# Kernel optimization log

Hardware: AMD Instinct MI355X
Metric: run time of the kernel (lower is better)

Reference implementation:

```python
import jax, jax.numpy as jnp
import numpy as np

N_ENT = 100000   # n_entities
N_HE = 20000     # n_hyperedges
D = 128          # in_dim == out_dim
NNZ_A = 3200000  # nnz of A_in (avg degree 32)
NNZ_H = 1000000  # nnz of each hyperedge incidence matrix


def spmm(rows, cols, vals, x, n_rows):
    """COO sparse (n_rows, n_cols) @ dense x (n_cols, d) -> (n_rows, d)."""
    return jax.ops.segment_sum(vals[:, None] * x[cols], rows, num_segments=n_rows)


def setup_inputs() -> dict:
    key = jax.random.key(0)
    ks = jax.random.split(key, 20)
    ri = lambda k, n, hi: jax.random.randint(k, (n,), 0, hi, dtype=jnp.int32)
    rv = lambda k, n: jax.random.uniform(k, (n,), dtype=jnp.float32) * 0.1
    inp = {
        "ego": jax.random.normal(ks[0], (N_ENT, D), dtype=jnp.float32),
        "A_rows": ri(ks[1], NNZ_A, N_ENT),
        "A_cols": ri(ks[2], NNZ_A, N_ENT),
        "A_vals": rv(ks[3], NNZ_A),
        "p1_rows": ri(ks[4], NNZ_H, N_HE),
        "p1_cols": ri(ks[5], NNZ_H, N_ENT),
        "p1_vals": rv(ks[6], NNZ_H),
        "p2_rows": ri(ks[7], NNZ_H, N_ENT),
        "p2_cols": ri(ks[8], NNZ_H, N_HE),
        "p2_vals": rv(ks[9], NNZ_H),
        "l1_rows": ri(ks[10], NNZ_H, N_HE),
        "l1_cols": ri(ks[11], NNZ_H, N_ENT),
        "l1_vals": rv(ks[12], NNZ_H),
        "l2_rows": ri(ks[13], NNZ_H, N_ENT),
        "l2_cols": ri(ks[14], NNZ_H, N_HE),
        "l2_vals": rv(ks[15], NNZ_H),
        "W1": jax.random.normal(ks[16], (D, D), dtype=jnp.float32) * (1.0 / np.sqrt(D)),
        "b1": jnp.zeros((D,), dtype=jnp.float32),
        "W2": jax.random.normal(ks[17], (D, D), dtype=jnp.float32) * (1.0 / np.sqrt(D)),
        "b2": jnp.zeros((D,), dtype=jnp.float32),
    }
    return inp


def reference(ego, A_rows, A_cols, A_vals,
              p1_rows, p1_cols, p1_vals, p2_rows, p2_cols, p2_vals,
              l1_rows, l1_cols, l1_vals, l2_rows, l2_cols, l2_vals,
              W1, b1, W2, b2):
    # side = A_in @ ego
    side = spmm(A_rows, A_cols, A_vals, ego, N_ENT)
    # proj = norm_proj2 @ (norm_proj1 @ ego)
    proj = spmm(p2_rows, p2_cols, p2_vals,
                spmm(p1_rows, p1_cols, p1_vals, ego, N_HE), N_ENT)
    # lib = norm_lib2 @ (norm_lib1 @ ego)
    lib = spmm(l2_rows, l2_cols, l2_vals,
               spmm(l1_rows, l1_cols, l1_vals, ego, N_HE), N_ENT)
    side = side + proj + lib
    # bi-interaction: LeakyReLU(Linear(ego+side)) + LeakyReLU(Linear(ego*side))
    sum_emb = jax.nn.leaky_relu((ego + side) @ W1.T + b1, negative_slope=0.01)
    bi_emb = jax.nn.leaky_relu((ego * side) @ W2.T + b2, negative_slope=0.01)
    # attention=True -> sum of both branches; message_dropout is identity in eval
    return sum_emb + bi_emb
```

## Files before the change

kernel.cpp:

```cpp
#include <hip/hip_runtime.h>

#define DIM 128
#define N_ENT 100000
#define N_HE  20000
#define NFE 1563
#define NFH 313
#define NFINE 2189
#define CAPF 3808
#define CAPH 3664
#define NCC 49
#define CAPC 110000
#define CHB 27
#define TA 4096
#define RPA 16
#define RPT 15

typedef __attribute__((ext_vector_type(8))) _Float16 f16x8;
typedef __attribute__((ext_vector_type(4))) _Float16 f16x4;
typedef __attribute__((ext_vector_type(4))) float f32x4;

__device__ __forceinline__ unsigned bf16_rne(float x) {
  unsigned b = __float_as_uint(x);
  return (b + 0x7fffu + ((b >> 16) & 1u)) >> 16;
}
__device__ __forceinline__ unsigned pack2(float lo, float hi) {
  return bf16_rne(lo) | (bf16_rne(hi) << 16);
}

__global__ __launch_bounds__(256) void cvt_bf16_kernel(const float* __restrict__ src,
                                                       unsigned* __restrict__ dst,
                                                       int n4) {
  for (int i = blockIdx.x * 256 + threadIdx.x; i < n4; i += gridDim.x * 256) {
    float4 v = reinterpret_cast<const float4*>(src)[i];
    reinterpret_cast<uint2*>(dst)[i] = make_uint2(pack2(v.x, v.y), pack2(v.z, v.w));
  }
}

__global__ __launch_bounds__(256) void cvt_f16_kernel(const float* __restrict__ src,
                                                      _Float16* __restrict__ dst, int n4) {
  for (int i = blockIdx.x * 256 + threadIdx.x; i < n4; i += gridDim.x * 256) {
    float4 v = reinterpret_cast<const float4*>(src)[i];
    f16x4 o;
    o.x = (_Float16)v.x;
    o.y = (_Float16)v.y;
    o.z = (_Float16)v.z;
    o.w = (_Float16)v.w;
    *reinterpret_cast<f16x4*>(dst + (size_t)i * 4) = o;
  }
}

struct SegB {
  const int* rows[5];
  const int* cols[5];
  const float* vals[5];
  int nnz[5];
  int blk_pfx[6];
};

__device__ __forceinline__ int seg_of(const int* pfx, int b) {
  int s = 0;
  while (s < 4 && b >= pfx[s + 1]) s++;
  return s;
}

__global__ __launch_bounds__(256) void binA_kernel(SegB a, int2* __restrict__ heapC,
                                                   int2* __restrict__ heapF,
                                                   int* __restrict__ gcurC,
                                                   int* __restrict__ gcurF) {
  __shared__ int2 srec[TA];
  __shared__ int s_cnt[NFH];
  __shared__ int s_delta[NFH];
  const int t = threadIdx.x;
  const int s = seg_of(a.blk_pfx, (int)blockIdx.x);
  const bool ent = (s < 3);
  const unsigned srctag = (s == 1) ? 1u : ((s == 2) ? 2u : 0u);
  const int heBase = (s == 3) ? NFE : (NFE + NFH);
  const int nbins = ent ? NCC : NFH;
  const int base = (blockIdx.x - a.blk_pfx[s]) * TA;
  const int cnt_here = min(TA, a.nnz[s] - base);
  const int* __restrict__ rows = a.rows[s];
  const int* __restrict__ cols = a.cols[s];
  const float* __restrict__ vals = a.vals[s];

  for (int i = t; i < nbins; i += 256) s_cnt[i] = 0;
  __syncthreads();

  uint2 rec[RPA];
#pragma unroll
  for (int j = 0; j < RPA; j++) {
    int li = t + j * 256;
    if (li < cnt_here) {
      int e = base + li;
      int r = rows[e];
      unsigned c = (unsigned)cols[e];
      unsigned vb = bf16_rne(vals[e]);
      if (ent) {
        int coarse = r >> 11;
        rec[j].x = c | (srctag << 17) | ((unsigned)(r & 63) << 19) |
                   ((unsigned)((r >> 6) & 31) << 25);
        rec[j].y = (vb << 16) | (unsigned)coarse;
        atomicAdd(&s_cnt[coarse], 1);
      } else {
        int fb = r >> 6;
        rec[j].x = c | ((unsigned)(r & 63) << 19);
        rec[j].y = (vb << 16) | (unsigned)fb;
        atomicAdd(&s_cnt[fb], 1);
      }
    }
  }
  __syncthreads();

  if (t == 0) {
    int run = 0;
    for (int i = 0; i < nbins; i++) { int v = s_cnt[i]; s_cnt[i] = run; run += v; }
  }
  __syncthreads();

  for (int i = t; i < nbins; i += 256) {
    int st = s_cnt[i];
    int en = (i == nbins - 1) ? cnt_here : s_cnt[i + 1];
    int c = en - st;
    if (c > 0) {
      if (ent) {
        int gb = atomicAdd(&gcurC[i], c);
        s_delta[i] = i * CAPC + gb - st;
      } else {
        int fg = heBase + i;
        int gb = atomicAdd(&gcurF[fg], c);
        s_delta[i] = fg * CAPF + gb - st;
      }
    }
  }
  __syncthreads();

#pragma unroll
  for (int j = 0; j < RPA; j++) {
    int li = t + j * 256;
    if (li < cnt_here) {
      int bin = ent ? (int)(rec[j].y & 63u) : (int)(rec[j].y & 0x1FFu);
      int p = atomicAdd(&s_cnt[bin], 1);
      srec[p] = make_int2((int)rec[j].x, (int)rec[j].y);
    }
  }
  __syncthreads();

  int2* __restrict__ heap = ent ? heapC : heapF;
  for (int i = t; i < cnt_here; i += 256) {
    int2 rr = srec[i];
    unsigned ry = (unsigned)rr.y;
    int bin = ent ? (int)(ry & 63u) : (int)(ry & 0x1FFu);
    int addr = s_delta[bin] + i;
    int rel = ent ? (addr - bin * CAPC) : (addr - (heBase + bin) * CAPF);
    int cap = ent ? CAPC : CAPF;
    if (rel < cap) heap[addr] = make_int2(rr.x, (int)(ry & 0xFFFF0000u));
  }
}

__global__ __launch_bounds__(256) void binB_kernel(const int2* __restrict__ heapC,
                                                   const int* __restrict__ gcurC,
                                                   int2* __restrict__ heapF,
                                                   int* __restrict__ gcurF) {
  __shared__ int2 srec[TA];
  __shared__ int s_cnt[32];
  __shared__ int s_delta[32];
  const int t = threadIdx.x;
  const int c = blockIdx.x / CHB;
  const int ch = blockIdx.x % CHB;
  const int ccnt = min(gcurC[c], CAPC);
  const int base = ch * TA;
  const int cnt_here = min(TA, ccnt - base);
  if (cnt_here <= 0) return;
  const int2* __restrict__ src = heapC + (size_t)c * CAPC + base;

  if (t < 32) s_cnt[t] = 0;
  __syncthreads();

  uint2 rec[RPA];
#pragma unroll
  for (int j = 0; j < RPA; j++) {
    int li = t + j * 256;
    if (li < cnt_here) {
      int2 v = src[li];
      rec[j] = make_uint2((unsigned)v.x, (unsigned)v.y);
      atomicAdd(&s_cnt[(rec[j].x >> 25) & 31u], 1);
    }
  }
  __syncthreads();

  if (t == 0) {
    int run = 0;
    for (int i = 0; i < 32; i++) { int v = s_cnt[i]; s_cnt[i] = run; run += v; }
  }
  __syncthreads();

  if (t < 32) {
    int st = s_cnt[t];
    int en = (t == 31) ? cnt_here : s_cnt[t + 1];
    int cc = en - st;
    if (cc > 0) {
      int fine = c * 32 + t;
      int gb = atomicAdd(&gcurF[fine], cc);
      s_delta[t] = fine * CAPF + gb - st;
    }
  }
  __syncthreads();

#pragma unroll
  for (int j = 0; j < RPA; j++) {
    int li = t + j * 256;
    if (li < cnt_here) {
      int bin = (int)((rec[j].x >> 25) & 31u);
      int p = atomicAdd(&s_cnt[bin], 1);
      srec[p] = make_int2((int)rec[j].x, (int)rec[j].y);
    }
  }
  __syncthreads();

  for (int i = t; i < cnt_here; i += 256) {
    int2 rr = srec[i];
    int bin = (int)(((unsigned)rr.x >> 25) & 31u);
    int addr = s_delta[bin] + i;
    int rel = addr - (c * 32 + bin) * CAPF;
    if (rel < CAPF)
      heapF[addr] = make_int2((int)((unsigned)rr.x & 0x01FFFFFFu), rr.y);
  }
}

__device__ __forceinline__ void bf16_fma4(float4& acc, uint2 g, float v) {
  acc.x = fmaf(v, __uint_as_float((g.x & 0xffffu) << 16), acc.x);
  acc.y = fmaf(v, __uint_as_float(g.x & 0xffff0000u), acc.y);
  acc.z = fmaf(v, __uint_as_float((g.y & 0xffffu) << 16), acc.z);
  acc.w = fmaf(v, __uint_as_float(g.y & 0xffff0000u), acc.w);
}

__global__ __launch_bounds__(256) void spmm_ent_kernel(
    const int2* __restrict__ heapF, const int* __restrict__ gcurF,
    const unsigned* __restrict__ x0, const unsigned* __restrict__ x1,
    const unsigned* __restrict__ x2, float* __restrict__ out) {
  __shared__ int2 srec[CAPF];
  __shared__ int sh_cnt[64];
  __shared__ int sh_off[65];
  __shared__ int sh_cur[64];
  const int b = blockIdx.x;
  const int t = threadIdx.x;
  const int cnt = min(gcurF[b], CAPF);
  const size_t base = (size_t)b * CAPF;

  if (t < 64) sh_cnt[t] = 0;
  __syncthreads();

  int2 rec[RPT];
#pragma unroll
  for (int j = 0; j < RPT; j++) {
    int idx = t + j * 256;
    if (idx < cnt) {
      rec[j] = heapF[base + idx];
      atomicAdd(&sh_cnt[((unsigned)rec[j].x) >> 19], 1);
    }
  }
  __syncthreads();

  if (t == 0) {
    int run = 0;
    for (int i = 0; i < 64; i++) { sh_off[i] = run; sh_cur[i] = run; run += sh_cnt[i]; }
    sh_off[64] = run;
  }
  __syncthreads();

#pragma unroll
  for (int j = 0; j < RPT; j++) {
    int idx = t + j * 256;
    if (idx < cnt) {
      int rl = (int)(((unsigned)rec[j].x) >> 19);
      int p = atomicAdd(&sh_cur[rl], 1);
      srec[p] = rec[j];
    }
  }
  __syncthreads();

  const int grp = t >> 5, sub = t & 31;
  const int row0 = b * 64;
  for (int r = grp; r < 64; r += 8) {
    int gr = row0 + r;
    if (gr >= N_ENT) continue;
    float4 acc = make_float4(0.f, 0.f, 0.f, 0.f);
    const int je = sh_off[r + 1];
    int j = sh_off[r];
    for (; j + 4 <= je; j += 4) {
      int2 r0 = srec[j], r1 = srec[j + 1], r2 = srec[j + 2], r3 = srec[j + 3];
      unsigned k0 = (unsigned)r0.x, k1 = (unsigned)r1.x, k2 = (unsigned)r2.x, k3 = (unsigned)r3.x;
      const unsigned* p0 = ((k0 >> 17) & 3u) == 0u ? x0 : (((k0 >> 17) & 3u) == 1u ? x1 : x2);
      const unsigned* p1 = ((k1 >> 17) & 3u) == 0u ? x0 : (((k1 >> 17) & 3u) == 1u ? x1 : x2);
      const unsigned* p2 = ((k2 >> 17) & 3u) == 0u ? x0 : (((k2 >> 17) & 3u) == 1u ? x1 : x2);
      const unsigned* p3 = ((k3 >> 17) & 3u) == 0u ? x0 : (((k3 >> 17) & 3u) == 1u ? x1 : x2);
      uint2 g0 = *reinterpret_cast<const uint2*>(p0 + (size_t)(k0 & 0x1FFFFu) * 64 + sub * 2);
      uint2 g1 = *reinterpret_cast<const uint2*>(p1 + (size_t)(k1 & 0x1FFFFu) * 64 + sub * 2);
      uint2 g2 = *reinterpret_cast<const uint2*>(p2 + (size_t)(k2 & 0x1FFFFu) * 64 + sub * 2);
      uint2 g3 = *reinterpret_cast<const uint2*>(p3 + (size_t)(k3 & 0x1FFFFu) * 64 + sub * 2);
      bf16_fma4(acc, g0, __int_as_float(r0.y));
      bf16_fma4(acc, g1, __int_as_float(r1.y));
      bf16_fma4(acc, g2, __int_as_float(r2.y));
      bf16_fma4(acc, g3, __int_as_float(r3.y));
    }
    for (; j < je; j++) {
      int2 rr = srec[j];
      unsigned k = (unsigned)rr.x;
      const unsigned* ph = ((k >> 17) & 3u) == 0u ? x0 : (((k >> 17) & 3u) == 1u ? x1 : x2);
      uint2 g = *reinterpret_cast<const uint2*>(ph + (size_t)(k & 0x1FFFFu) * 64 + sub * 2);
      bf16_fma4(acc, g, __int_as_float(rr.y));
    }
    *reinterpret_cast<float4*>(out + (size_t)gr * DIM + sub * 4) = acc;
  }
}

__global__ __launch_bounds__(256) void spmm_he_kernel(
    const int2* __restrict__ heapF, const int* __restrict__ gcurF,
    const unsigned* __restrict__ egoh,
    unsigned* __restrict__ tmp1h, unsigned* __restrict__ tmp2h) {
  __shared__ int2 srec[CAPH];
  __shared__ int sh_cnt[64];
  __shared__ int sh_off[65];
  __shared__ int sh_cur[64];
  const int half = blockIdx.x >= NFH;
  const int b = half ? (int)blockIdx.x - NFH : (int)blockIdx.x;
  const int fine = (half ? NFE + NFH : NFE) + b;
  unsigned* outh = half ? tmp2h : tmp1h;
  const int t = threadIdx.x;
  const int cnt = min(gcurF[fine], CAPH);
  const size_t base = (size_t)fine * CAPF;

  if (t < 64) sh_cnt[t] = 0;
  __syncthreads();

  int2 rec[RPT];
#pragma unroll
  for (int j = 0; j < RPT; j++) {
    int idx = t + j * 256;
    if (idx < cnt) {
      rec[j] = heapF[base + idx];
      atomicAdd(&sh_cnt[((unsigned)rec[j].x) >> 19], 1);
    }
  }
  __syncthreads();

  if (t == 0) {
    int run = 0;
    for (int i = 0; i < 64; i++) { sh_off[i] = run; sh_cur[i] = run; run += sh_cnt[i]; }
    sh_off[64] = run;
  }
  __syncthreads();

#pragma unroll
  for (int j = 0; j < RPT; j++) {
    int idx = t + j * 256;
    if (idx < cnt) {
      int rl = (int)(((unsigned)rec[j].x) >> 19);
      int p = atomicAdd(&sh_cur[rl], 1);
      srec[p] = rec[j];
    }
  }
  __syncthreads();

  const int grp = t >> 5, sub = t & 31;
  const int row0 = b * 64;
  for (int r = grp; r < 64; r += 8) {
    int gr = row0 + r;
    if (gr >= N_HE) continue;
    float4 acc = make_float4(0.f, 0.f, 0.f, 0.f);
    const int je = sh_off[r + 1];
    int j = sh_off[r];
    for (; j + 4 <= je; j += 4) {
      int2 r0 = srec[j], r1 = srec[j + 1], r2 = srec[j + 2], r3 = srec[j + 3];
      uint2 g0 = *reinterpret_cast<const uint2*>(egoh + (size_t)(((unsigned)r0.x) & 0x1FFFFu) * 64 + sub * 2);
      uint2 g1 = *reinterpret_cast<const uint2*>(egoh + (size_t)(((unsigned)r1.x) & 0x1FFFFu) * 64 + sub * 2);
      uint2 g2 = *reinterpret_cast<const uint2*>(egoh + (size_t)(((unsigned)r2.x) & 0x1FFFFu) * 64 + sub * 2);
      uint2 g3 = *reinterpret_cast<const uint2*>(egoh + (size_t)(((unsigned)r3.x) & 0x1FFFFu) * 64 + sub * 2);
      bf16_fma4(acc, g0, __int_as_float(r0.y));
      bf16_fma4(acc, g1, __int_as_float(r1.y));
      bf16_fma4(acc, g2, __int_as_float(r2.y));
      bf16_fma4(acc, g3, __int_as_float(r3.y));
    }
    for (; j < je; j++) {
      int2 rr = srec[j];
      uint2 g = *reinterpret_cast<const uint2*>(egoh + (size_t)(((unsigned)rr.x) & 0x1FFFFu) * 64 + sub * 2);
      bf16_fma4(acc, g, __int_as_float(rr.y));
    }
    *reinterpret_cast<uint2*>(outh + (size_t)gr * 64 + sub * 2) =
        make_uint2(pack2(acc.x, acc.y), pack2(acc.z, acc.w));
  }
}

__device__ __forceinline__ float lrelu(float v) { return v > 0.0f ? v : 0.01f * v; }

__global__ __launch_bounds__(256, 3) void mfma_epilogue_kernel(
    const float* __restrict__ ego,
    float* __restrict__ out,
    const _Float16* __restrict__ w1h,
    const _Float16* __restrict__ w2h,
    const float* __restrict__ b1,
    const float* __restrict__ b2) {
  __shared__ __align__(16) _Float16 s_sum[64 * DIM];
  __shared__ __align__(16) _Float16 s_prod[64 * DIM];
  const int t = threadIdx.x;
  const int row0 = blockIdx.x * 64;

  for (int i = t; i < 64 * (DIM / 4); i += 256) {
    int r = i >> 5;
    int c4 = (i & 31) * 4;
    int gr = row0 + r;
    float4 e4 = make_float4(0.f, 0.f, 0.f, 0.f);
    float4 sd4 = make_float4(0.f, 0.f, 0.f, 0.f);
    if (gr < N_ENT) {
      e4 = *reinterpret_cast<const float4*>(ego + (size_t)gr * DIM + c4);
      sd4 = *reinterpret_cast<const float4*>(out + (size_t)gr * DIM + c4);
    }
    int sidx = (r * DIM + c4) ^ ((r & 7) << 3);
    f16x4 sv, pv;
    sv.x = (_Float16)(e4.x + sd4.x);
    sv.y = (_Float16)(e4.y + sd4.y);
    sv.z = (_Float16)(e4.z + sd4.z);
    sv.w = (_Float16)(e4.w + sd4.w);
    pv.x = (_Float16)(e4.x * sd4.x);
    pv.y = (_Float16)(e4.y * sd4.y);
    pv.z = (_Float16)(e4.z * sd4.z);
    pv.w = (_Float16)(e4.w * sd4.w);
    *reinterpret_cast<f16x4*>(&s_sum[sidx]) = sv;
    *reinterpret_cast<f16x4*>(&s_prod[sidx]) = pv;
  }
  __syncthreads();

  const int w = t >> 6;
  const int l = t & 63;
  const int lr = l & 15;
  const int lk = l >> 4;

  f32x4 acc1[8] = {};
  f32x4 acc2[8] = {};

#pragma unroll
  for (int ks = 0; ks < 4; ks++) {
    int arow = w * 16 + lr;
    int sidx = (arow * DIM + ks * 32 + lk * 8) ^ ((arow & 7) << 3);
    f16x8 a1 = *reinterpret_cast<const f16x8*>(&s_sum[sidx]);
    f16x8 a2 = *reinterpret_cast<const f16x8*>(&s_prod[sidx]);
#pragma unroll
    for (int jt = 0; jt < 8; jt++) {
      int fidx = (jt * 16 + lr) * DIM + ks * 32 + lk * 8;
      f16x8 bw1 = *reinterpret_cast<const f16x8*>(w1h + fidx);
      f16x8 bw2 = *reinterpret_cast<const f16x8*>(w2h + fidx);
      acc1[jt] = __builtin_amdgcn_mfma_f32_16x16x32_f16(a1, bw1, acc1[jt], 0, 0, 0);
      acc2[jt] = __builtin_amdgcn_mfma_f32_16x16x32_f16(a2, bw2, acc2[jt], 0, 0, 0);
    }
  }

#pragma unroll
  for (int jt = 0; jt < 8; jt++) {
    int col = jt * 16 + lr;
    float bb1 = b1[col];
    float bb2 = b2[col];
#pragma unroll
    for (int r = 0; r < 4; r++) {
      int gr = row0 + w * 16 + lk * 4 + r;
      if (gr < N_ENT)
        out[(size_t)gr * DIM + col] = lrelu(acc1[jt][r] + bb1) + lrelu(acc2[jt][r] + bb2);
    }
  }
}

extern "C" void kernel_launch(void* const* d_in, const int* in_sizes, int n_in,
                              void* d_out, int out_size, void* d_ws, size_t ws_size,
                              hipStream_t stream) {
  const float* ego     = (const float*)d_in[0];
  const float* W1      = (const float*)d_in[16];
  const float* b1      = (const float*)d_in[17];
  const float* W2      = (const float*)d_in[18];
  const float* b2      = (const float*)d_in[19];

  int2* heapF = (int2*)d_ws;
  int2* heapC = heapF + (size_t)NFINE * CAPF;
  int*  gcurC = (int*)(heapC + (size_t)NCC * CAPC);
  int*  gcurF = gcurC + NCC;
  unsigned* egoh  = (unsigned*)heapC;
  unsigned* tmp1h = egoh + (size_t)N_ENT * 64;
  unsigned* tmp2h = tmp1h + (size_t)N_HE * 64;
  _Float16* w1h = (_Float16*)(tmp2h + (size_t)N_HE * 64);
  _Float16* w2h = w1h + DIM * DIM;

  hipMemsetAsync(gcurC, 0, (size_t)(NCC + NFINE) * sizeof(int), stream);

  SegB sg;
  sg.rows[0] = (const int*)d_in[1];  sg.cols[0] = (const int*)d_in[2];  sg.vals[0] = (const float*)d_in[3];  sg.nnz[0] = in_sizes[1];
  sg.rows[1] = (const int*)d_in[7];  sg.cols[1] = (const int*)d_in[8];  sg.vals[1] = (const float*)d_in[9];  sg.nnz[1] = in_sizes[7];
  sg.rows[2] = (const int*)d_in[13]; sg.cols[2] = (const int*)d_in[14]; sg.vals[2] = (const float*)d_in[15]; sg.nnz[2] = in_sizes[13];
  sg.rows[3] = (const int*)d_in[4];  sg.cols[3] = (const int*)d_in[5];  sg.vals[3] = (const float*)d_in[6];  sg.nnz[3] = in_sizes[4];
  sg.rows[4] = (const int*)d_in[10]; sg.cols[4] = (const int*)d_in[11]; sg.vals[4] = (const float*)d_in[12]; sg.nnz[4] = in_sizes[10];
  int pfx = 0;
  for (int s = 0; s < 5; s++) {
    sg.blk_pfx[s] = pfx;
    pfx += (sg.nnz[s] + TA - 1) / TA;
  }
  sg.blk_pfx[5] = pfx;

  binA_kernel<<<dim3(pfx), dim3(256), 0, stream>>>(sg, heapC, heapF, gcurC, gcurF);
  binB_kernel<<<dim3(NCC * CHB), dim3(256), 0, stream>>>(heapC, gcurC, heapF, gcurF);

  cvt_bf16_kernel<<<dim3(2048), dim3(256), 0, stream>>>(ego, egoh, N_ENT * (DIM / 4));
  cvt_f16_kernel<<<dim3(16), dim3(256), 0, stream>>>(W1, w1h, DIM * DIM / 4);
  cvt_f16_kernel<<<dim3(16), dim3(256), 0, stream>>>(W2, w2h, DIM * DIM / 4);

  float* side = (float*)d_out;

  spmm_he_kernel<<<dim3(2 * NFH), dim3(256), 0, stream>>>(heapF, gcurF, egoh, tmp1h, tmp2h);
  spmm_ent_kernel<<<dim3(NFE), dim3(256), 0, stream>>>(heapF, gcurF, egoh, tmp1h, tmp2h, side);
  mfma_epilogue_kernel<<<dim3((N_ENT + 63) / 64), dim3(256), 0, stream>>>(
      ego, side, w1h, w2h, b1, b2);
}
```

Before: 471.8 us.

## Fuse entity SpMM with MFMA bi-interaction epilogue and unify gather source indexing

```diff
diff --git a/kernel.cpp b/kernel.cpp
--- a/kernel.cpp
+++ b/kernel.cpp
@@ -26,6 +26,12 @@
 __device__ __forceinline__ unsigned pack2(float lo, float hi) {
   return bf16_rne(lo) | (bf16_rne(hi) << 16);
 }
+__device__ __forceinline__ unsigned packh2(float lo, float hi) {
+  union { _Float16 h[2]; unsigned u; } cv;
+  cv.h[0] = (_Float16)lo;
+  cv.h[1] = (_Float16)hi;
+  return cv.u;
+}
 
 __global__ __launch_bounds__(256) void cvt_bf16_kernel(const float* __restrict__ src,
                                                        unsigned* __restrict__ dst,
@@ -41,10 +47,7 @@
   for (int i = blockIdx.x * 256 + threadIdx.x; i < n4; i += gridDim.x * 256) {
     float4 v = reinterpret_cast<const float4*>(src)[i];
     f16x4 o;
-    o.x = (_Float16)v.x;
-    o.y = (_Float16)v.y;
-    o.z = (_Float16)v.z;
-    o.w = (_Float16)v.w;
+    o.x = (_Float16)v.x; o.y = (_Float16)v.y; o.z = (_Float16)v.z; o.w = (_Float16)v.w;
     *reinterpret_cast<f16x4*>(dst + (size_t)i * 4) = o;
   }
 }
@@ -73,7 +76,7 @@
   const int t = threadIdx.x;
   const int s = seg_of(a.blk_pfx, (int)blockIdx.x);
   const bool ent = (s < 3);
-  const unsigned srctag = (s == 1) ? 1u : ((s == 2) ? 2u : 0u);
+  const unsigned cbase = (s == 1) ? 100000u : ((s == 2) ? 120000u : 0u);
   const int heBase = (s == 3) ? NFE : (NFE + NFH);
   const int nbins = ent ? NCC : NFH;
   const int base = (blockIdx.x - a.blk_pfx[s]) * TA;
@@ -92,19 +95,16 @@
     if (li < cnt_here) {
       int e = base + li;
       int r = rows[e];
-      unsigned c = (unsigned)cols[e];
       unsigned vb = bf16_rne(vals[e]);
       if (ent) {
-        int coarse = r >> 11;
-        rec[j].x = c | (srctag << 17) | ((unsigned)(r & 63) << 19) |
-                   ((unsigned)((r >> 6) & 31) << 25);
-        rec[j].y = (vb << 16) | (unsigned)coarse;
-        atomicAdd(&s_cnt[coarse], 1);
+        unsigned ccol = (unsigned)cols[e] + cbase;
+        rec[j].x = (unsigned)(r & 63) | (ccol << 6) | ((unsigned)((r >> 6) & 31) << 24);
+        rec[j].y = (vb << 16) | (unsigned)(r >> 11);
+        atomicAdd(&s_cnt[r >> 11], 1);
       } else {
-        int fb = r >> 6;
-        rec[j].x = c | ((unsigned)(r & 63) << 19);
-        rec[j].y = (vb << 16) | (unsigned)fb;
-        atomicAdd(&s_cnt[fb], 1);
+        rec[j].x = (unsigned)(r & 63) | ((unsigned)cols[e] << 6);
+        rec[j].y = (vb << 16) | (unsigned)(r >> 6);
+        atomicAdd(&s_cnt[r >> 6], 1);
       }
     }
   }
@@ -182,7 +182,7 @@
     if (li < cnt_here) {
       int2 v = src[li];
       rec[j] = make_uint2((unsigned)v.x, (unsigned)v.y);
-      atomicAdd(&s_cnt[(rec[j].x >> 25) & 31u], 1);
+      atomicAdd(&s_cnt[(rec[j].x >> 24) & 31u], 1);
     }
   }
   __syncthreads();
@@ -209,7 +209,7 @@
   for (int j = 0; j < RPA; j++) {
     int li = t + j * 256;
     if (li < cnt_here) {
-      int bin = (int)((rec[j].x >> 25) & 31u);
+      int bin = (int)((rec[j].x >> 24) & 31u);
       int p = atomicAdd(&s_cnt[bin], 1);
       srec[p] = make_int2((int)rec[j].x, (int)rec[j].y);
     }
@@ -218,29 +218,38 @@
 
   for (int i = t; i < cnt_here; i += 256) {
     int2 rr = srec[i];
-    int bin = (int)(((unsigned)rr.x >> 25) & 31u);
+    int bin = (int)(((unsigned)rr.x >> 24) & 31u);
     int addr = s_delta[bin] + i;
     int rel = addr - (c * 32 + bin) * CAPF;
     if (rel < CAPF)
-      heapF[addr] = make_int2((int)((unsigned)rr.x & 0x01FFFFFFu), rr.y);
+      heapF[addr] = make_int2((int)((unsigned)rr.x & 0x00FFFFFFu), rr.y);
   }
 }
 
 __device__ __forceinline__ void bf16_fma4(float4& acc, uint2 g, float v) {
-  acc.x = fmaf(v, __uint_as_float((g.x & 0xffffu) << 16), acc.x);
+  acc.x = fmaf(v, __uint_as_float(g.x << 16), acc.x);
   acc.y = fmaf(v, __uint_as_float(g.x & 0xffff0000u), acc.y);
-  acc.z = fmaf(v, __uint_as_float((g.y & 0xffffu) << 16), acc.z);
+  acc.z = fmaf(v, __uint_as_float(g.y << 16), acc.z);
   acc.w = fmaf(v, __uint_as_float(g.y & 0xffff0000u), acc.w);
 }
 
-__global__ __launch_bounds__(256) void spmm_ent_kernel(
+__device__ __forceinline__ float lrelu(float v) { return v > 0.0f ? v : 0.01f * v; }
+
+__global__ __launch_bounds__(256) void spmm_ent_fused_kernel(
     const int2* __restrict__ heapF, const int* __restrict__ gcurF,
-    const unsigned* __restrict__ x0, const unsigned* __restrict__ x1,
-    const unsigned* __restrict__ x2, float* __restrict__ out) {
-  __shared__ int2 srec[CAPF];
+    const unsigned* __restrict__ xall,
+    const float* __restrict__ ego,
+    const _Float16* __restrict__ w1h, const _Float16* __restrict__ w2h,
+    const float* __restrict__ b1, const float* __restrict__ b2,
+    float* __restrict__ out) {
+  __shared__ __align__(16) char smem[32768];
   __shared__ int sh_cnt[64];
   __shared__ int sh_off[65];
   __shared__ int sh_cur[64];
+  int2* srec = (int2*)smem;
+  _Float16* s_sum = (_Float16*)smem;
+  _Float16* s_prod = (_Float16*)(smem + 16384);
+
   const int b = blockIdx.x;
   const int t = threadIdx.x;
   const int cnt = min(gcurF[b], CAPF);
@@ -255,7 +264,7 @@
     int idx = t + j * 256;
     if (idx < cnt) {
       rec[j] = heapF[base + idx];
-      atomicAdd(&sh_cnt[((unsigned)rec[j].x) >> 19], 1);
+      atomicAdd(&sh_cnt[((unsigned)rec[j].x) & 63u], 1);
     }
   }
   __syncthreads();
@@ -271,7 +280,7 @@
   for (int j = 0; j < RPT; j++) {
     int idx = t + j * 256;
     if (idx < cnt) {
-      int rl = (int)(((unsigned)rec[j].x) >> 19);
+      int rl = (int)(((unsigned)rec[j].x) & 63u);
       int p = atomicAdd(&sh_cur[rl], 1);
       srec[p] = rec[j];
     }
@@ -280,23 +289,20 @@
 
   const int grp = t >> 5, sub = t & 31;
   const int row0 = b * 64;
-  for (int r = grp; r < 64; r += 8) {
-    int gr = row0 + r;
-    if (gr >= N_ENT) continue;
+  uint2 sreg[8], preg[8];
+#pragma unroll
+  for (int i = 0; i < 8; i++) {
+    const int r = grp + i * 8;
+    const int gr = row0 + r;
     float4 acc = make_float4(0.f, 0.f, 0.f, 0.f);
     const int je = sh_off[r + 1];
     int j = sh_off[r];
     for (; j + 4 <= je; j += 4) {
       int2 r0 = srec[j], r1 = srec[j + 1], r2 = srec[j + 2], r3 = srec[j + 3];
-      unsigned k0 = (unsigned)r0.x, k1 = (unsigned)r1.x, k2 = (unsigned)r2.x, k3 = (unsigned)r3.x;
-      const unsigned* p0 = ((k0 >> 17) & 3u) == 0u ? x0 : (((k0 >> 17) & 3u) == 1u ? x1 : x2);
-      const unsigned* p1 = ((k1 >> 17) & 3u) == 0u ? x0 : (((k1 >> 17) & 3u) == 1u ? x1 : x2);
-      const unsigned* p2 = ((k2 >> 17) & 3u) == 0u ? x0 : (((k2 >> 17) & 3u) == 1u ? x1 : x2);
-      const unsigned* p3 = ((k3 >> 17) & 3u) == 0u ? x0 : (((k3 >> 17) & 3u) == 1u ? x1 : x2);
-      uint2 g0 = *reinterpret_cast<const uint2*>(p0 + (size_t)(k0 & 0x1FFFFu) * 64 + sub * 2);
-      uint2 g1 = *reinterpret_cast<const uint2*>(p1 + (size_t)(k1 & 0x1FFFFu) * 64 + sub * 2);
-      uint2 g2 = *reinterpret_cast<const uint2*>(p2 + (size_t)(k2 & 0x1FFFFu) * 64 + sub * 2);
-      uint2 g3 = *reinterpret_cast<const uint2*>(p3 + (size_t)(k3 & 0x1FFFFu) * 64 + sub * 2);
+      uint2 g0 = *reinterpret_cast<const uint2*>(xall + (((unsigned)r0.x) & 0xFFFFC0u) + sub * 2);
+      uint2 g1 = *reinterpret_cast<const uint2*>(xall + (((unsigned)r1.x) & 0xFFFFC0u) + sub * 2);
+      uint2 g2 = *reinterpret_cast<const uint2*>(xall + (((unsigned)r2.x) & 0xFFFFC0u) + sub * 2);
+      uint2 g3 = *reinterpret_cast<const uint2*>(xall + (((unsigned)r3.x) & 0xFFFFC0u) + sub * 2);
       bf16_fma4(acc, g0, __int_as_float(r0.y));
       bf16_fma4(acc, g1, __int_as_float(r1.y));
       bf16_fma4(acc, g2, __int_as_float(r2.y));
@@ -304,12 +310,60 @@
     }
     for (; j < je; j++) {
       int2 rr = srec[j];
-      unsigned k = (unsigned)rr.x;
-      const unsigned* ph = ((k >> 17) & 3u) == 0u ? x0 : (((k >> 17) & 3u) == 1u ? x1 : x2);
-      uint2 g = *reinterpret_cast<const uint2*>(ph + (size_t)(k & 0x1FFFFu) * 64 + sub * 2);
+      uint2 g = *reinterpret_cast<const uint2*>(xall + (((unsigned)rr.x) & 0xFFFFC0u) + sub * 2);
       bf16_fma4(acc, g, __int_as_float(rr.y));
     }
-    *reinterpret_cast<float4*>(out + (size_t)gr * DIM + sub * 4) = acc;
+    float4 e4 = make_float4(0.f, 0.f, 0.f, 0.f);
+    if (gr < N_ENT) e4 = *reinterpret_cast<const float4*>(ego + (size_t)gr * DIM + sub * 4);
+    sreg[i] = make_uint2(packh2(e4.x + acc.x, e4.y + acc.y), packh2(e4.z + acc.z, e4.w + acc.w));
+    preg[i] = make_uint2(packh2(e4.x * acc.x, e4.y * acc.y), packh2(e4.z * acc.z, e4.w * acc.w));
+  }
+  __syncthreads();
+
+#pragma unroll
+  for (int i = 0; i < 8; i++) {
+    const int r = grp + i * 8;
+    int sidx = (r * DIM + sub * 4) ^ ((r & 7) << 3);
+    *reinterpret_cast<uint2*>(&s_sum[sidx]) = sreg[i];
+    *reinterpret_cast<uint2*>(&s_prod[sidx]) = preg[i];
+  }
+  __syncthreads();
+
+  const int w = t >> 6;
+  const int l = t & 63;
+  const int lr = l & 15;
+  const int lk = l >> 4;
+
+  f32x4 acc1[8] = {};
+  f32x4 acc2[8] = {};
+
+#pragma unroll
+  for (int ks = 0; ks < 4; ks++) {
+    int arow = w * 16 + lr;
+    int sidx = (arow * DIM + ks * 32 + lk * 8) ^ ((arow & 7) << 3);
+    f16x8 a1 = *reinterpret_cast<const f16x8*>(&s_sum[sidx]);
+    f16x8 a2 = *reinterpret_cast<const f16x8*>(&s_prod[sidx]);
+#pragma unroll
+    for (int jt = 0; jt < 8; jt++) {
+      int fidx = (jt * 16 + lr) * DIM + ks * 32 + lk * 8;
+      f16x8 bw1 = *reinterpret_cast<const f16x8*>(w1h + fidx);
+      f16x8 bw2 = *reinterpret_cast<const f16x8*>(w2h + fidx);
+      acc1[jt] = __builtin_amdgcn_mfma_f32_16x16x32_f16(a1, bw1, acc1[jt], 0, 0, 0);
+      acc2[jt] = __builtin_amdgcn_mfma_f32_16x16x32_f16(a2, bw2, acc2[jt], 0, 0, 0);
+    }
+  }
+
+#pragma unroll
+  for (int jt = 0; jt < 8; jt++) {
+    int col = jt * 16 + lr;
+    float bb1 = b1[col];
+    float bb2 = b2[col];
+#pragma unroll
+    for (int r = 0; r < 4; r++) {
+      int gr = row0 + w * 16 + lk * 4 + r;
+      if (gr < N_ENT)
+        out[(size_t)gr * DIM + col] = lrelu(acc1[jt][r] + bb1) + lrelu(acc2[jt][r] + bb2);
+    }
   }
 }
 
@@ -338,7 +392,7 @@
     int idx = t + j * 256;
     if (idx < cnt) {
       rec[j] = heapF[base + idx];
-      atomicAdd(&sh_cnt[((unsigned)rec[j].x) >> 19], 1);
+      atomicAdd(&sh_cnt[((unsigned)rec[j].x) & 63u], 1);
     }
   }
   __syncthreads();
@@ -354,7 +408,7 @@
   for (int j = 0; j < RPT; j++) {
     int idx = t + j * 256;
     if (idx < cnt) {
-      int rl = (int)(((unsigned)rec[j].x) >> 19);
+      int rl = (int)(((unsigned)rec[j].x) & 63u);
       int p = atomicAdd(&sh_cur[rl], 1);
       srec[p] = rec[j];
     }
@@ -371,10 +425,10 @@
     int j = sh_off[r];
     for (; j + 4 <= je; j += 4) {
       int2 r0 = srec[j], r1 = srec[j + 1], r2 = srec[j + 2], r3 = srec[j + 3];
-      uint2 g0 = *reinterpret_cast<const uint2*>(egoh + (size_t)(((unsigned)r0.x) & 0x1FFFFu) * 64 + sub * 2);
-      uint2 g1 = *reinterpret_cast<const uint2*>(egoh + (size_t)(((unsigned)r1.x) & 0x1FFFFu) * 64 + sub * 2);
-      uint2 g2 = *reinterpret_cast<const uint2*>(egoh + (size_t)(((unsigned)r2.x) & 0x1FFFFu) * 64 + sub * 2);
-      uint2 g3 = *reinterpret_cast<const uint2*>(egoh + (size_t)(((unsigned)r3.x) & 0x1FFFFu) * 64 + sub * 2);
+      uint2 g0 = *reinterpret_cast<const uint2*>(egoh + (((unsigned)r0.x) & 0xFFFFC0u) + sub * 2);
+      uint2 g1 = *reinterpret_cast<const uint2*>(egoh + (((unsigned)r1.x) & 0xFFFFC0u) + sub * 2);
+      uint2 g2 = *reinterpret_cast<const uint2*>(egoh + (((unsigned)r2.x) & 0xFFFFC0u) + sub * 2);
+      uint2 g3 = *reinterpret_cast<const uint2*>(egoh + (((unsigned)r3.x) & 0xFFFFC0u) + sub * 2);
       bf16_fma4(acc, g0, __int_as_float(r0.y));
       bf16_fma4(acc, g1, __int_as_float(r1.y));
       bf16_fma4(acc, g2, __int_as_float(r2.y));
@@ -382,88 +436,11 @@
     }
     for (; j < je; j++) {
       int2 rr = srec[j];
-      uint2 g = *reinterpret_cast<const uint2*>(egoh + (size_t)(((unsigned)rr.x) & 0x1FFFFu) * 64 + sub * 2);
+      uint2 g = *reinterpret_cast<const uint2*>(egoh + (((unsigned)rr.x) & 0xFFFFC0u) + sub * 2);
       bf16_fma4(acc, g, __int_as_float(rr.y));
     }
     *reinterpret_cast<uint2*>(outh + (size_t)gr * 64 + sub * 2) =
         make_uint2(pack2(acc.x, acc.y), pack2(acc.z, acc.w));
-  }
-}
-
-__device__ __forceinline__ float lrelu(float v) { return v > 0.0f ? v : 0.01f * v; }
-
-__global__ __launch_bounds__(256, 3) void mfma_epilogue_kernel(
-    const float* __restrict__ ego,
-    float* __restrict__ out,
-    const _Float16* __restrict__ w1h,
-    const _Float16* __restrict__ w2h,
-    const float* __restrict__ b1,
-    const float* __restrict__ b2) {
-  __shared__ __align__(16) _Float16 s_sum[64 * DIM];
-  __shared__ __align__(16) _Float16 s_prod[64 * DIM];
-  const int t = threadIdx.x;
-  const int row0 = blockIdx.x * 64;
-
-  for (int i = t; i < 64 * (DIM / 4); i += 256) {
-    int r = i >> 5;
-    int c4 = (i & 31) * 4;
-    int gr = row0 + r;
-    float4 e4 = make_float4(0.f, 0.f, 0.f, 0.f);
-    float4 sd4 = make_float4(0.f, 0.f, 0.f, 0.f);
-    if (gr < N_ENT) {
-      e4 = *reinterpret_cast<const float4*>(ego + (size_t)gr * DIM + c4);
-      sd4 = *reinterpret_cast<const float4*>(out + (size_t)gr * DIM + c4);
-    }
-    int sidx = (r * DIM + c4) ^ ((r & 7) << 3);
-    f16x4 sv, pv;
-    sv.x = (_Float16)(e4.x + sd4.x);
-    sv.y = (_Float16)(e4.y + sd4.y);
-    sv.z = (_Float16)(e4.z + sd4.z);
-    sv.w = (_Float16)(e4.w + sd4.w);
-    pv.x = (_Float16)(e4.x * sd4.x);
-    pv.y = (_Float16)(e4.y * sd4.y);
-    pv.z = (_Float16)(e4.z * sd4.z);
-    pv.w = (_Float16)(e4.w * sd4.w);
-    *reinterpret_cast<f16x4*>(&s_sum[sidx]) = sv;
-    *reinterpret_cast<f16x4*>(&s_prod[sidx]) = pv;
-  }
-  __syncthreads();
-
-  const int w = t >> 6;
-  const int l = t & 63;
-  const int lr = l & 15;
-  const int lk = l >> 4;
-
-  f32x4 acc1[8] = {};
-  f32x4 acc2[8] = {};
-
-#pragma unroll
-  for (int ks = 0; ks < 4; ks++) {
-    int arow = w * 16 + lr;
-    int sidx = (arow * DIM + ks * 32 + lk * 8) ^ ((arow & 7) << 3);
-    f16x8 a1 = *reinterpret_cast<const f16x8*>(&s_sum[sidx]);
-    f16x8 a2 = *reinterpret_cast<const f16x8*>(&s_prod[sidx]);
-#pragma unroll
-    for (int jt = 0; jt < 8; jt++) {
-      int fidx = (jt * 16 + lr) * DIM + ks * 32 + lk * 8;
-      f16x8 bw1 = *reinterpret_cast<const f16x8*>(w1h + fidx);
-      f16x8 bw2 = *reinterpret_cast<const f16x8*>(w2h + fidx);
-      acc1[jt] = __builtin_amdgcn_mfma_f32_16x16x32_f16(a1, bw1, acc1[jt], 0, 0, 0);
-      acc2[jt] = __builtin_amdgcn_mfma_f32_16x16x32_f16(a2, bw2, acc2[jt], 0, 0, 0);
-    }
-  }
-
-#pragma unroll
-  for (int jt = 0; jt < 8; jt++) {
-    int col = jt * 16 + lr;
-    float bb1 = b1[col];
-    float bb2 = b2[col];
-#pragma unroll
-    for (int r = 0; r < 4; r++) {
-      int gr = row0 + w * 16 + lk * 4 + r;
-      if (gr < N_ENT)
-        out[(size_t)gr * DIM + col] = lrelu(acc1[jt][r] + bb1) + lrelu(acc2[jt][r] + bb2);
-    }
   }
 }
 
@@ -508,10 +485,7 @@
   cvt_f16_kernel<<<dim3(16), dim3(256), 0, stream>>>(W1, w1h, DIM * DIM / 4);
   cvt_f16_kernel<<<dim3(16), dim3(256), 0, stream>>>(W2, w2h, DIM * DIM / 4);
 
-  float* side = (float*)d_out;
-
   spmm_he_kernel<<<dim3(2 * NFH), dim3(256), 0, stream>>>(heapF, gcurF, egoh, tmp1h, tmp2h);
-  spmm_ent_kernel<<<dim3(NFE), dim3(256), 0, stream>>>(heapF, gcurF, egoh, tmp1h, tmp2h, side);
-  mfma_epilogue_kernel<<<dim3((N_ENT + 63) / 64), dim3(256), 0, stream>>>(
-      ego, side, w1h, w2h, b1, b2);
-}
+  spmm_ent_fused_kernel<<<dim3(NFE), dim3(256), 0, stream>>>(
+      heapF, gcurF, egoh, ego, w1h, w2h, b1, b2, (float*)d_out);
+}
```

Result: slower. 502.5 us (+6.5%).

## Halve fine bin size, compact LDS records, and pre-scale gather addresses

Applied to the files above, without the earlier changes.

```diff
diff --git a/kernel.cpp b/kernel.cpp
--- a/kernel.cpp
+++ b/kernel.cpp
@@ -3,17 +3,16 @@
 #define DIM 128
 #define N_ENT 100000
 #define N_HE  20000
-#define NFE 1563
-#define NFH 313
-#define NFINE 2189
-#define CAPF 3808
-#define CAPH 3664
+#define NFE 3125
+#define NFH 625
+#define NFINE 4375
+#define CAPF 2000
 #define NCC 49
 #define CAPC 110000
 #define CHB 27
 #define TA 4096
 #define RPA 16
-#define RPT 15
+#define RPT 8
 
 typedef __attribute__((ext_vector_type(8))) _Float16 f16x8;
 typedef __attribute__((ext_vector_type(4))) _Float16 f16x4;
@@ -41,10 +40,7 @@
   for (int i = blockIdx.x * 256 + threadIdx.x; i < n4; i += gridDim.x * 256) {
     float4 v = reinterpret_cast<const float4*>(src)[i];
     f16x4 o;
-    o.x = (_Float16)v.x;
-    o.y = (_Float16)v.y;
-    o.z = (_Float16)v.z;
-    o.w = (_Float16)v.w;
+    o.x = (_Float16)v.x; o.y = (_Float16)v.y; o.z = (_Float16)v.z; o.w = (_Float16)v.w;
     *reinterpret_cast<f16x4*>(dst + (size_t)i * 4) = o;
   }
 }
@@ -73,7 +69,7 @@
   const int t = threadIdx.x;
   const int s = seg_of(a.blk_pfx, (int)blockIdx.x);
   const bool ent = (s < 3);
-  const unsigned srctag = (s == 1) ? 1u : ((s == 2) ? 2u : 0u);
+  const unsigned cbase = (s == 1) ? 100000u : ((s == 2) ? 120000u : 0u);
   const int heBase = (s == 3) ? NFE : (NFE + NFH);
   const int nbins = ent ? NCC : NFH;
   const int base = (blockIdx.x - a.blk_pfx[s]) * TA;
@@ -92,19 +88,16 @@
     if (li < cnt_here) {
       int e = base + li;
       int r = rows[e];
-      unsigned c = (unsigned)cols[e];
       unsigned vb = bf16_rne(vals[e]);
       if (ent) {
-        int coarse = r >> 11;
-        rec[j].x = c | (srctag << 17) | ((unsigned)(r & 63) << 19) |
-                   ((unsigned)((r >> 6) & 31) << 25);
-        rec[j].y = (vb << 16) | (unsigned)coarse;
-        atomicAdd(&s_cnt[coarse], 1);
+        unsigned ccol = (unsigned)cols[e] + cbase;
+        rec[j].x = (unsigned)(r & 31) | (ccol << 6) | ((unsigned)((r >> 5) & 63) << 24);
+        rec[j].y = (vb << 16) | (unsigned)(r >> 11);
+        atomicAdd(&s_cnt[r >> 11], 1);
       } else {
-        int fb = r >> 6;
-        rec[j].x = c | ((unsigned)(r & 63) << 19);
-        rec[j].y = (vb << 16) | (unsigned)fb;
-        atomicAdd(&s_cnt[fb], 1);
+        rec[j].x = (unsigned)(r & 31) | ((unsigned)cols[e] << 6);
+        rec[j].y = (vb << 16) | (unsigned)(r >> 5);
+        atomicAdd(&s_cnt[r >> 5], 1);
       }
     }
   }
@@ -137,7 +130,7 @@
   for (int j = 0; j < RPA; j++) {
     int li = t + j * 256;
     if (li < cnt_here) {
-      int bin = ent ? (int)(rec[j].y & 63u) : (int)(rec[j].y & 0x1FFu);
+      int bin = ent ? (int)(rec[j].y & 63u) : (int)(rec[j].y & 0x3FFu);
       int p = atomicAdd(&s_cnt[bin], 1);
       srec[p] = make_int2((int)rec[j].x, (int)rec[j].y);
     }
@@ -148,7 +141,7 @@
   for (int i = t; i < cnt_here; i += 256) {
     int2 rr = srec[i];
     unsigned ry = (unsigned)rr.y;
-    int bin = ent ? (int)(ry & 63u) : (int)(ry & 0x1FFu);
+    int bin = ent ? (int)(ry & 63u) : (int)(ry & 0x3FFu);
     int addr = s_delta[bin] + i;
     int rel = ent ? (addr - bin * CAPC) : (addr - (heBase + bin) * CAPF);
     int cap = ent ? CAPC : CAPF;
@@ -161,8 +154,8 @@
                                                    int2* __restrict__ heapF,
                                                    int* __restrict__ gcurF) {
   __shared__ int2 srec[TA];
-  __shared__ int s_cnt[32];
-  __shared__ int s_delta[32];
+  __shared__ int s_cnt[64];
+  __shared__ int s_delta[64];
   const int t = threadIdx.x;
   const int c = blockIdx.x / CHB;
   const int ch = blockIdx.x % CHB;
@@ -172,7 +165,7 @@
   if (cnt_here <= 0) return;
   const int2* __restrict__ src = heapC + (size_t)c * CAPC + base;
 
-  if (t < 32) s_cnt[t] = 0;
+  if (t < 64) s_cnt[t] = 0;
   __syncthreads();
 
   uint2 rec[RPA];
@@ -182,23 +175,23 @@
     if (li < cnt_here) {
       int2 v = src[li];
       rec[j] = make_uint2((unsigned)v.x, (unsigned)v.y);
-      atomicAdd(&s_cnt[(rec[j].x >> 25) & 31u], 1);
+      atomicAdd(&s_cnt[(rec[j].x >> 24) & 63u], 1);
     }
   }
   __syncthreads();
 
   if (t == 0) {
     int run = 0;
-    for (int i = 0; i < 32; i++) { int v = s_cnt[i]; s_cnt[i] = run; run += v; }
-  }
-  __syncthreads();
-
-  if (t < 32) {
+    for (int i = 0; i < 64; i++) { int v = s_cnt[i]; s_cnt[i] = run; run += v; }
+  }
+  __syncthreads();
+
+  if (t < 64) {
     int st = s_cnt[t];
-    int en = (t == 31) ? cnt_here : s_cnt[t + 1];
+    int en = (t == 63) ? cnt_here : s_cnt[t + 1];
     int cc = en - st;
     if (cc > 0) {
-      int fine = c * 32 + t;
+      int fine = c * 64 + t;
       int gb = atomicAdd(&gcurF[fine], cc);
       s_delta[t] = fine * CAPF + gb - st;
     }
@@ -209,7 +202,7 @@
   for (int j = 0; j < RPA; j++) {
     int li = t + j * 256;
     if (li < cnt_here) {
-      int bin = (int)((rec[j].x >> 25) & 31u);
+      int bin = (int)((rec[j].x >> 24) & 63u);
       int p = atomicAdd(&s_cnt[bin], 1);
       srec[p] = make_int2((int)rec[j].x, (int)rec[j].y);
     }
@@ -218,35 +211,37 @@
 
   for (int i = t; i < cnt_here; i += 256) {
     int2 rr = srec[i];
-    int bin = (int)(((unsigned)rr.x >> 25) & 31u);
+    int bin = (int)(((unsigned)rr.x >> 24) & 63u);
     int addr = s_delta[bin] + i;
-    int rel = addr - (c * 32 + bin) * CAPF;
+    int rel = addr - (c * 64 + bin) * CAPF;
     if (rel < CAPF)
-      heapF[addr] = make_int2((int)((unsigned)rr.x & 0x01FFFFFFu), rr.y);
+      heapF[addr] = make_int2((int)((unsigned)rr.x & 0x00FFFFFFu), rr.y);
   }
 }
 
 __device__ __forceinline__ void bf16_fma4(float4& acc, uint2 g, float v) {
-  acc.x = fmaf(v, __uint_as_float((g.x & 0xffffu) << 16), acc.x);
+  acc.x = fmaf(v, __uint_as_float(g.x << 16), acc.x);
   acc.y = fmaf(v, __uint_as_float(g.x & 0xffff0000u), acc.y);
-  acc.z = fmaf(v, __uint_as_float((g.y & 0xffffu) << 16), acc.z);
+  acc.z = fmaf(v, __uint_as_float(g.y << 16), acc.z);
   acc.w = fmaf(v, __uint_as_float(g.y & 0xffff0000u), acc.w);
 }
 
-__global__ __launch_bounds__(256) void spmm_ent_kernel(
+__device__ __forceinline__ float lrelu(float v) { return v > 0.0f ? v : 0.01f * v; }
+
+__global__ __launch_bounds__(256, 8) void spmm_ent_kernel(
     const int2* __restrict__ heapF, const int* __restrict__ gcurF,
-    const unsigned* __restrict__ x0, const unsigned* __restrict__ x1,
-    const unsigned* __restrict__ x2, float* __restrict__ out) {
-  __shared__ int2 srec[CAPF];
-  __shared__ int sh_cnt[64];
-  __shared__ int sh_off[65];
-  __shared__ int sh_cur[64];
+    const unsigned* __restrict__ xall, float* __restrict__ out) {
+  __shared__ unsigned skey[CAPF];
+  __shared__ unsigned short sval[CAPF];
+  __shared__ int sh_cnt[32];
+  __shared__ int sh_off[33];
+  __shared__ int sh_cur[32];
   const int b = blockIdx.x;
   const int t = threadIdx.x;
   const int cnt = min(gcurF[b], CAPF);
   const size_t base = (size_t)b * CAPF;
 
-  if (t < 64) sh_cnt[t] = 0;
+  if (t < 32) sh_cnt[t] = 0;
   __syncthreads();
 
   int2 rec[RPT];
@@ -255,15 +250,15 @@
     int idx = t + j * 256;
     if (idx < cnt) {
       rec[j] = heapF[base + idx];
-      atomicAdd(&sh_cnt[((unsigned)rec[j].x) >> 19], 1);
+      atomicAdd(&sh_cnt[((unsigned)rec[j].x) & 31u], 1);
     }
   }
   __syncthreads();
 
   if (t == 0) {
     int run = 0;
-    for (int i = 0; i < 64; i++) { sh_off[i] = run; sh_cur[i] = run; run += sh_cnt[i]; }
-    sh_off[64] = run;
+    for (int i = 0; i < 32; i++) { sh_off[i] = run; sh_cur[i] = run; run += sh_cnt[i]; }
+    sh_off[32] = run;
   }
   __syncthreads();
 
@@ -271,65 +266,65 @@
   for (int j = 0; j < RPT; j++) {
     int idx = t + j * 256;
     if (idx < cnt) {
-      int rl = (int)(((unsigned)rec[j].x) >> 19);
+      int rl = (int)(((unsigned)rec[j].x) & 31u);
       int p = atomicAdd(&sh_cur[rl], 1);
-      srec[p] = rec[j];
+      skey[p] = (unsigned)rec[j].x;
+      sval[p] = (unsigned short)((unsigned)rec[j].y >> 16);
     }
   }
   __syncthreads();
 
   const int grp = t >> 5, sub = t & 31;
-  const int row0 = b * 64;
-  for (int r = grp; r < 64; r += 8) {
-    int gr = row0 + r;
-    if (gr >= N_ENT) continue;
+  const int row0 = b * 32;
+#pragma unroll
+  for (int i = 0; i < 4; i++) {
+    const int r = grp + i * 8;
     float4 acc = make_float4(0.f, 0.f, 0.f, 0.f);
     const int je = sh_off[r + 1];
     int j = sh_off[r];
     for (; j + 4 <= je; j += 4) {
-      int2 r0 = srec[j], r1 = srec[j + 1], r2 = srec[j + 2], r3 = srec[j + 3];
-      unsigned k0 = (unsigned)r0.x, k1 = (unsigned)r1.x, k2 = (unsigned)r2.x, k3 = (unsigned)r3.x;
-      const unsigned* p0 = ((k0 >> 17) & 3u) == 0u ? x0 : (((k0 >> 17) & 3u) == 1u ? x1 : x2);
-      const unsigned* p1 = ((k1 >> 17) & 3u) == 0u ? x0 : (((k1 >> 17) & 3u) == 1u ? x1 : x2);
-      const unsigned* p2 = ((k2 >> 17) & 3u) == 0u ? x0 : (((k2 >> 17) & 3u) == 1u ? x1 : x2);
-      const unsigned* p3 = ((k3 >> 17) & 3u) == 0u ? x0 : (((k3 >> 17) & 3u) == 1u ? x1 : x2);
-      uint2 g0 = *reinterpret_cast<const uint2*>(p0 + (size_t)(k0 & 0x1FFFFu) * 64 + sub * 2);
-      uint2 g1 = *reinterpret_cast<const uint2*>(p1 + (size_t)(k1 & 0x1FFFFu) * 64 + sub * 2);
-      uint2 g2 = *reinterpret_cast<const uint2*>(p2 + (size_t)(k2 & 0x1FFFFu) * 64 + sub * 2);
-      uint2 g3 = *reinterpret_cast<const uint2*>(p3 + (size_t)(k3 & 0x1FFFFu) * 64 + sub * 2);
-      bf16_fma4(acc, g0, __int_as_float(r0.y));
-      bf16_fma4(acc, g1, __int_as_float(r1.y));
-      bf16_fma4(acc, g2, __int_as_float(r2.y));
-      bf16_fma4(acc, g3, __int_as_float(r3.y));
+      unsigned k0 = skey[j], k1 = skey[j + 1], k2 = skey[j + 2], k3 = skey[j + 3];
+      float v0 = __uint_as_float((unsigned)sval[j] << 16);
+      float v1 = __uint_as_float((unsigned)sval[j + 1] << 16);
+      float v2 = __uint_as_float((unsigned)sval[j + 2] << 16);
+      float v3 = __uint_as_float((unsigned)sval[j + 3] << 16);
+      uint2 g0 = *reinterpret_cast<const uint2*>(xall + (k0 & 0x00FFFFC0u) + sub * 2);
+      uint2 g1 = *reinterpret_cast<const uint2*>(xall + (k1 & 0x00FFFFC0u) + sub * 2);
+      uint2 g2 = *reinterpret_cast<const uint2*>(xall + (k2 & 0x00FFFFC0u) + sub * 2);
+      uint2 g3 = *reinterpret_cast<const uint2*>(xall + (k3 & 0x00FFFFC0u) + sub * 2);
+      bf16_fma4(acc, g0, v0);
+      bf16_fma4(acc, g1, v1);
+      bf16_fma4(acc, g2, v2);
+      bf16_fma4(acc, g3, v3);
     }
     for (; j < je; j++) {
-      int2 rr = srec[j];
-      unsigned k = (unsigned)rr.x;
-      const unsigned* ph = ((k >> 17) & 3u) == 0u ? x0 : (((k >> 17) & 3u) == 1u ? x1 : x2);
-      uint2 g = *reinterpret_cast<const uint2*>(ph + (size_t)(k & 0x1FFFFu) * 64 + sub * 2);
-      bf16_fma4(acc, g, __int_as_float(rr.y));
-    }
-    *reinterpret_cast<float4*>(out + (size_t)gr * DIM + sub * 4) = acc;
-  }
-}
-
-__global__ __launch_bounds__(256) void spmm_he_kernel(
+      unsigned k = skey[j];
+      float v = __uint_as_float((unsigned)sval[j] << 16);
+      uint2 g = *reinterpret_cast<const uint2*>(xall + (k & 0x00FFFFC0u) + sub * 2);
+      bf16_fma4(acc, g, v);
+    }
+    *reinterpret_cast<float4*>(out + (size_t)(row0 + r) * DIM + sub * 4) = acc;
+  }
+}
+
+__global__ __launch_bounds__(256, 8) void spmm_he_kernel(
     const int2* __restrict__ heapF, const int* __restrict__ gcurF,
     const unsigned* __restrict__ egoh,
     unsigned* __restrict__ tmp1h, unsigned* __restrict__ tmp2h) {
-  __shared__ int2 srec[CAPH];
-  __shared__ int sh_cnt[64];
-  __shared__ int sh_off[65];
-  __shared__ int sh_cur[64];
+  __shared__ unsigned skey[CAPF];
+  __shared__ unsigned short sval[CAPF];
+  __shared__ int sh_cnt[32];
+  __shared__ int sh_off[33];
+  __shared__ int sh_cur[32];
   const int half = blockIdx.x >= NFH;
   const int b = half ? (int)blockIdx.x - NFH : (int)blockIdx.x;
   const int fine = (half ? NFE + NFH : NFE) + b;
   unsigned* outh = half ? tmp2h : tmp1h;
   const int t = threadIdx.x;
-  const int cnt = min(gcurF[fine], CAPH);
+  const int cnt = min(gcurF[fine], CAPF);
   const size_t base = (size_t)fine * CAPF;
 
-  if (t < 64) sh_cnt[t] = 0;
+  if (t < 32) sh_cnt[t] = 0;
   __syncthreads();
 
   int2 rec[RPT];
@@ -338,15 +333,15 @@
     int idx = t + j * 256;
     if (idx < cnt) {
       rec[j] = heapF[base + idx];
-      atomicAdd(&sh_cnt[((unsigned)rec[j].x) >> 19], 1);
+      atomicAdd(&sh_cnt[((unsigned)rec[j].x) & 31u], 1);
     }
   }
   __syncthreads();
 
   if (t == 0) {
     int run = 0;
-    for (int i = 0; i < 64; i++) { sh_off[i] = run; sh_cur[i] = run; run += sh_cnt[i]; }
-    sh_off[64] = run;
+    for (int i = 0; i < 32; i++) { sh_off[i] = run; sh_cur[i] = run; run += sh_cnt[i]; }
+    sh_off[32] = run;
   }
   __syncthreads();
 
@@ -354,43 +349,47 @@
   for (int j = 0; j < RPT; j++) {
     int idx = t + j * 256;
     if (idx < cnt) {
-      int rl = (int)(((unsigned)rec[j].x) >> 19);
+      int rl = (int)(((unsigned)rec[j].x) & 31u);
       int p = atomicAdd(&sh_cur[rl], 1);
-      srec[p] = rec[j];
+      skey[p] = (unsigned)rec[j].x;
+      sval[p] = (unsigned short)((unsigned)rec[j].y >> 16);
     }
   }
   __syncthreads();
 
   const int grp = t >> 5, sub = t & 31;
-  const int row0 = b * 64;
-  for (int r = grp; r < 64; r += 8) {
-    int gr = row0 + r;
-    if (gr >= N_HE) continue;
+  const int row0 = b * 32;
+#pragma unroll
+  for (int i = 0; i < 4; i++) {
+    const int r = grp + i * 8;
     float4 acc = make_float4(0.f, 0.f, 0.f, 0.f);
     const int je = sh_off[r + 1];
     int j = sh_off[r];
     for (; j + 4 <= je; j += 4) {
-      int2 r0 = srec[j], r1 = srec[j + 1], r2 = srec[j + 2], r3 = srec[j + 3];
-      uint2 g0 = *reinterpret_cast<const uint2*>(egoh + (size_t)(((unsigned)r0.x) & 0x1FFFFu) * 64 + sub * 2);
-      uint2 g1 = *reinterpret_cast<const uint2*>(egoh + (size_t)(((unsigned)r1.x) & 0x1FFFFu) * 64 + sub * 2);
-      uint2 g2 = *reinterpret_cast<const uint2*>(egoh + (size_t)(((unsigned)r2.x) & 0x1FFFFu) * 64 + sub * 2);
-      uint2 g3 = *reinterpret_cast<const uint2*>(egoh + (size_t)(((unsigned)r3.x) & 0x1FFFFu) * 64 + sub * 2);
-      bf16_fma4(acc, g0, __int_as_float(r0.y));
-      bf16_fma4(acc, g1, __int_as_float(r1.y));
-      bf16_fma4(acc, g2, __int_as_float(r2.y));
-      bf16_fma4(acc, g3, __int_as_float(r3.y));
+      unsigned k0 = skey[j], k1 = skey[j + 1], k2 = skey[j + 2], k3 = skey[j + 3];
+      float v0 = __uint_as_float((unsigned)sval[j] << 16);
+      float v1 = __uint_as_float((unsigned)sval[j + 1] << 16);
+      float v2 = __uint_as_float((unsigned)sval[j + 2] << 16);
+      float v3 = __uint_as_float((unsigned)sval[j + 3] << 16);
+      uint2 g0 = *reinterpret_cast<const uint2*>(egoh + (k0 & 0x00FFFFC0u) + sub * 2);
+      uint2 g1 = *reinterpret_cast<const uint2*>(egoh + (k1 & 0x00FFFFC0u) + sub * 2);
+      uint2 g2 = *reinterpret_cast<const uint2*>(egoh + (k2 & 0x00FFFFC0u) + sub * 2);
+      uint2 g3 = *reinterpret_cast<const uint2*>(egoh + (k3 & 0x00FFFFC0u) + sub * 2);
+      bf16_fma4(acc, g0, v0);
+      bf16_fma4(acc, g1, v1);
+      bf16_fma4(acc, g2, v2);
+      bf16_fma4(acc, g3, v3);
     }
     for (; j < je; j++) {
-      int2 rr = srec[j];
-      uint2 g = *reinterpret_cast<const uint2*>(egoh + (size_t)(((unsigned)rr.x) & 0x1FFFFu) * 64 + sub * 2);
-      bf16_fma4(acc, g, __int_as_float(rr.y));
-    }
-    *reinterpret_cast<uint2*>(outh + (size_t)gr * 64 + sub * 2) =
+      unsigned k = skey[j];
+      float v = __uint_as_float((unsigned)sval[j] << 16);
+      uint2 g = *reinterpret_cast<const uint2*>(egoh + (k & 0x00FFFFC0u) + sub * 2);
+      bf16_fma4(acc, g, v);
+    }
+    *reinterpret_cast<uint2*>(outh + (size_t)(row0 + r) * 64 + sub * 2) =
         make_uint2(pack2(acc.x, acc.y), pack2(acc.z, acc.w));
   }
 }
-
-__device__ __forceinline__ float lrelu(float v) { return v > 0.0f ? v : 0.01f * v; }
 
 __global__ __launch_bounds__(256, 3) void mfma_epilogue_kernel(
     const float* __restrict__ ego,
@@ -511,7 +510,7 @@
   float* side = (float*)d_out;
 
   spmm_he_kernel<<<dim3(2 * NFH), dim3(256), 0, stream>>>(heapF, gcurF, egoh, tmp1h, tmp2h);
-  spmm_ent_kernel<<<dim3(NFE), dim3(256), 0, stream>>>(heapF, gcurF, egoh, tmp1h, tmp2h, side);
+  spmm_ent_kernel<<<dim3(NFE), dim3(256), 0, stream>>>(heapF, gcurF, egoh, side);
   mfma_epilogue_kernel<<<dim3((N_ENT + 63) / 64), dim3(256), 0, stream>>>(
       ego, side, w1h, w2h, b1, b2);
 }
```

After: 447.4 us. -5.2%, faster.
